# Performance work log

Hardware: AMD Instinct MI355X
Metric: run time of the kernel (lower is better)

## Reference

```python
import jax, jax.numpy as jnp
import numpy as np

V, D, L, ITERS, B, S = 30522, 256, 4, 10, 256, 512
UPDATE_RATE = 0.1


def _lin(x, w, b):
    # torch nn.Linear: y = x @ W^T + b, w: [out, in]
    return jnp.matmul(x, w.T) + b


def setup_inputs() -> dict:
    key = jax.random.key(0)
    ks = jax.random.split(key, 20)
    s = 0.02
    inp = {
        "input_ids": jax.random.randint(ks[0], (B, S), 0, V),
        "embedding": jax.random.normal(ks[1], (V, D), jnp.float32) * s,
        "pos_enc": jax.random.normal(ks[2], (1, S, D), jnp.float32) * s,
        # stacked per-layer PredictiveCodingLayer params [L, ...]
        "init_w": jax.random.normal(ks[3], (L, D, D), jnp.float32) * s,
        "init_b": jnp.zeros((L, D), jnp.float32),
        "pred_w": jax.random.normal(ks[4], (L, D, D), jnp.float32) * s,
        "pred_b": jnp.zeros((L, D), jnp.float32),
        "upd_w": jax.random.normal(ks[5], (L, D, D), jnp.float32) * s,
        "upd_b": jnp.zeros((L, D), jnp.float32),
        "start_q_w": jax.random.normal(ks[6], (D, D), jnp.float32) * s,
        "start_q_b": jnp.zeros((D,), jnp.float32),
        "end_q_w": jax.random.normal(ks[7], (D, D), jnp.float32) * s,
        "end_q_b": jnp.zeros((D,), jnp.float32),
        "key_w": jax.random.normal(ks[8], (D, D), jnp.float32) * s,
        "key_b": jnp.zeros((D,), jnp.float32),
        "ans_w1": jax.random.normal(ks[9], (D // 2, D), jnp.float32) * s,
        "ans_b1": jnp.zeros((D // 2,), jnp.float32),
        "ans_w2": jax.random.normal(ks[10], (2, D // 2), jnp.float32) * s,
        "ans_b2": jnp.zeros((2,), jnp.float32),
    }
    return inp


def reference(input_ids, embedding, pos_enc, init_w, init_b, pred_w, pred_b,
              upd_w, upd_b, start_q_w, start_q_b, end_q_w, end_q_b,
              key_w, key_b, ans_w1, ans_b1, ans_w2, ans_b2):
    seq_len = input_ids.shape[1]
    embeds = embedding[input_ids] + pos_enc[:, :seq_len, :]   # [B,S,D]
    pooled = jnp.mean(embeds, axis=1)                          # [B,D]

    predict = lambda i, r: _lin(r, pred_w[i], pred_b[i])

    # init_representation: tanh(Linear(x)) chained across layers
    reps = []
    cur = pooled
    for i in range(L):
        cur = jnp.tanh(_lin(cur, init_w[i], init_b[i]))
        reps.append(cur)
    ff_output = reps[-1]

    # iterative predictive-coding refinement
    for _ in range(ITERS):
        errors = [pooled - predict(0, reps[0])]
        for i in range(1, L):
            errors.append(jax.lax.stop_gradient(reps[i - 1]) - predict(i, reps[i]))
        new_reps = []
        for i in range(L):
            if i < L - 1:  # bidirectional
                error_above = reps[i] - predict(i + 1, reps[i + 1])
            else:
                error_above = jnp.zeros_like(reps[i])
            total_error = errors[i] + 0.5 * error_above
            # update: rep + rate * tanh(Linear(error))
            new_reps.append(reps[i] + UPDATE_RATE * jnp.tanh(_lin(total_error, upd_w[i], upd_b[i])))
        reps = new_reps

    refined = reps[-1] + ff_output                             # [B,D]
    token_keys = _lin(embeds, key_w, key_b)                    # [B,S,D]
    start_q = _lin(refined, start_q_w, start_q_b)
    end_q = _lin(refined, end_q_w, end_q_b)
    start_logits = jnp.einsum('bd,bsd->bs', start_q, token_keys)
    end_logits = jnp.einsum('bd,bsd->bs', end_q, token_keys)
    h = jax.nn.gelu(_lin(refined, ans_w1, ans_b1), approximate=False)
    answerable_logits = _lin(h, ans_w2, ans_b2)                # [B,2]
    return (start_logits, end_logits, answerable_logits)
```

## Files before the change

kernel.cpp:

```cpp
#include <hip/hip_runtime.h>
#include <math.h>

#define NB 256
#define NS 512
#define ND 256
#define NL 4
#define NITERS 10
#define DD (ND*ND)
#define BSTR 780
#define ASTR 132

__global__ __launch_bounds__(256) void k_pool1(const int* __restrict__ ids,
                                               const float* __restrict__ emb,
                                               const float* __restrict__ pos,
                                               float* __restrict__ partial) {
    const int bid = blockIdx.x;
    const int b = bid >> 2, q = bid & 3;
    const int t = threadIdx.x;
    __shared__ int sid[128];
    if (t < 128) sid[t] = ids[b * NS + q * 128 + t];
    __syncthreads();
    float acc = 0.f;
#pragma unroll 8
    for (int s = 0; s < 128; ++s)
        acc += emb[(size_t)sid[s] * ND + t] + pos[(q * 128 + s) * ND + t];
    partial[bid * ND + t] = acc;
}

__global__ __launch_bounds__(256) void k_prep(
    const float* __restrict__ pred_w, const float* __restrict__ pred_b,
    const float* __restrict__ upd_w,  const float* __restrict__ upd_b,
    const float* __restrict__ init_w,
    const float* __restrict__ sw, const float* __restrict__ sb,
    const float* __restrict__ ew, const float* __restrict__ eb,
    const float* __restrict__ kw, const float* __restrict__ kb,
    const float* __restrict__ w1,
    const float* __restrict__ partial,
    float* __restrict__ CM, float* __restrict__ CMI,
    float* __restrict__ KSt, float* __restrict__ KEt, float* __restrict__ W1t,
    float* __restrict__ cvec, float* __restrict__ rc0,
    float* __restrict__ vsk, float* __restrict__ vse,
    float* __restrict__ ksb, float* __restrict__ keb, float* __restrict__ scal)
{
    const int bid = blockIdx.x;
    const int t = threadIdx.x;

    if (bid < 576 || (bid >= 1056 && bid < 1120)) {
        int id, tile;
        if (bid < 576) { id = bid >> 6; tile = bid & 63; }
        else           { id = 9;        tile = bid - 1056; }
        const float* Asrc = nullptr; const float* Bsrc = nullptr;
        float alpha = 1.f, tau = 0.f; float* outp = nullptr;
        bool bT = false, aPool = false;
        switch (id) {
            case 0: Asrc = pred_w;        Bsrc = upd_w;        alpha=-1.f;  tau=0.5f; outp = CM + 0*(size_t)DD; break;
            case 1: Asrc = pred_w + DD;   Bsrc = upd_w;        alpha=-0.5f;           outp = CM + 1*(size_t)DD; break;
            case 2: Asrc = pred_w + DD;   Bsrc = upd_w + DD;   alpha=-1.f;  tau=0.5f; outp = CM + 4*(size_t)DD; break;
            case 3: Asrc = pred_w + 2*DD; Bsrc = upd_w + DD;   alpha=-0.5f;           outp = CM + 5*(size_t)DD; break;
            case 4: Asrc = pred_w + 2*DD; Bsrc = upd_w + 2*DD; alpha=-1.f;  tau=0.5f; outp = CM + 7*(size_t)DD; break;
            case 5: Asrc = pred_w + 3*DD; Bsrc = upd_w + 2*DD; alpha=-0.5f;           outp = CM + 8*(size_t)DD; break;
            case 6: Asrc = pred_w + 3*DD; Bsrc = upd_w + 3*DD; alpha=-1.f;            outp = CM + 10*(size_t)DD; break;
            case 7: Asrc = sw; Bsrc = kw; bT = true; outp = KSt; break;
            case 8: Asrc = ew; Bsrc = kw; bT = true; outp = KEt; break;
            default: Bsrc = upd_w; aPool = true; outp = rc0; break;
        }
        const float* Tsrc = (tau != 0.f) ? Bsrc : nullptr;
        const int i0 = (tile >> 3) * 32, j0 = (tile & 7) * 32;
        __shared__ float As[32 * 33];
        __shared__ float Bs[32 * 33];
        const int tx = t & 15, ty = t >> 4;
        float a00 = 0.f, a01 = 0.f, a10 = 0.f, a11 = 0.f;
        for (int e0 = 0; e0 < 256; e0 += 32) {
            __syncthreads();
            if (!aPool) {
                const int ii = t & 31, e8 = t >> 5;
#pragma unroll
                for (int p = 0; p < 4; ++p) {
                    int ee = e8 + 8 * p;
                    As[ee * 33 + ii] = Asrc[(size_t)(e0 + ee) * 256 + i0 + ii];
                }
            } else {
                const int ee = t & 31, i8 = t >> 5;
#pragma unroll
                for (int p = 0; p < 4; ++p) {
                    int ii = i8 + 8 * p;
                    const float* pp = partial + (size_t)(i0 + ii) * 4 * 256 + e0 + ee;
                    As[ee * 33 + ii] = (pp[0] + pp[256] + pp[512] + pp[768]) * (1.f / 512.f);
                }
            }
            if (!bT) {
                const int ee = t & 31, j8 = t >> 5;
#pragma unroll
                for (int p = 0; p < 4; ++p) {
                    int jj = j8 + 8 * p;
                    Bs[ee * 33 + jj] = Bsrc[(size_t)(j0 + jj) * 256 + e0 + ee];
                }
            } else {
                const int jj = t & 31, e8 = t >> 5;
#pragma unroll
                for (int p = 0; p < 4; ++p) {
                    int ee = e8 + 8 * p;
                    Bs[ee * 33 + jj] = Bsrc[(size_t)(e0 + ee) * 256 + j0 + jj];
                }
            }
            __syncthreads();
#pragma unroll
            for (int e = 0; e < 32; ++e) {
                float va0 = As[e * 33 + 2 * ty], va1 = As[e * 33 + 2 * ty + 1];
                float vb0 = Bs[e * 33 + 2 * tx], vb1 = Bs[e * 33 + 2 * tx + 1];
                a00 += va0 * vb0; a01 += va0 * vb1;
                a10 += va1 * vb0; a11 += va1 * vb1;
            }
        }
        float t00 = 0.f, t01 = 0.f, t10 = 0.f, t11 = 0.f;
        if (Tsrc) {
            t00 = Tsrc[(size_t)(j0 + 2 * tx) * 256 + i0 + 2 * ty];
            t01 = Tsrc[(size_t)(j0 + 2 * tx + 1) * 256 + i0 + 2 * ty];
            t10 = Tsrc[(size_t)(j0 + 2 * tx) * 256 + i0 + 2 * ty + 1];
            t11 = Tsrc[(size_t)(j0 + 2 * tx + 1) * 256 + i0 + 2 * ty + 1];
        }
        outp[(size_t)(i0 + 2 * ty) * 256 + j0 + 2 * tx]         = alpha * a00 + tau * t00;
        outp[(size_t)(i0 + 2 * ty) * 256 + j0 + 2 * tx + 1]     = alpha * a01 + tau * t01;
        outp[(size_t)(i0 + 2 * ty + 1) * 256 + j0 + 2 * tx]     = alpha * a10 + tau * t10;
        outp[(size_t)(i0 + 2 * ty + 1) * 256 + j0 + 2 * tx + 1] = alpha * a11 + tau * t11;
        return;
    }

    if (bid < 1024) {
        const int tid = bid - 576;
        const int m = tid >> 6, tile = tid & 63;
        const float* src; float* dst;
        if (m < 3) { src = upd_w + (size_t)(m + 1) * DD; dst = CM + (size_t)(3 + 3 * m) * DD; }
        else       { src = init_w + (size_t)(m - 3) * DD; dst = CMI + (size_t)(m - 3) * DD; }
        const int r0 = (tile >> 3) * 32, c0 = (tile & 7) * 32;
        __shared__ float T[32 * 33];
        const int cc = t & 31, r8 = t >> 5;
#pragma unroll
        for (int p = 0; p < 4; ++p) {
            int rr = r8 + 8 * p;
            T[rr * 33 + cc] = src[(size_t)(r0 + rr) * 256 + c0 + cc];
        }
        __syncthreads();
#pragma unroll
        for (int p = 0; p < 4; ++p) {
            int rr = r8 + 8 * p;
            dst[(size_t)(c0 + rr) * 256 + r0 + cc] = T[cc * 33 + rr];
        }
        return;
    }

    if (bid < 1056) {
        const int tile = bid - 1024;
        const int e0 = (tile >> 2) * 32, j0 = (tile & 3) * 32;
        __shared__ float T[32 * 33];
        const int cc = t & 31, r8 = t >> 5;
#pragma unroll
        for (int p = 0; p < 4; ++p) {
            int jj = r8 + 8 * p;
            T[jj * 33 + cc] = w1[(size_t)(j0 + jj) * 256 + e0 + cc];
        }
        __syncthreads();
#pragma unroll
        for (int p = 0; p < 4; ++p) {
            int ee = r8 + 8 * p;
            W1t[(size_t)(e0 + ee) * 128 + j0 + cc] = T[cc * 33 + ee];
        }
        return;
    }

    const int vb = bid - 1120;
    if (vb < 4) {
        const int l = vb;
        __shared__ float v[256];
        v[t] = (l < 3) ? pred_b[l * 256 + t] + 0.5f * pred_b[(l + 1) * 256 + t]
                       : pred_b[3 * 256 + t];
        __syncthreads();
        const float* U = upd_w + (size_t)l * DD + (size_t)t * 256;
        float acc = 0.f;
#pragma unroll 8
        for (int k = 0; k < 256; k += 4) {
            float4 u = *(const float4*)&U[k];
            acc += u.x * v[k] + u.y * v[k + 1] + u.z * v[k + 2] + u.w * v[k + 3];
        }
        cvec[l * 256 + t] = upd_b[l * 256 + t] - acc;
        return;
    }
    {
        const float* W = (vb == 4) ? sw : ew;
        const float* bb = (vb == 4) ? sb : eb;
        float* vout = (vb == 4) ? vsk : vse;
        float* bout = (vb == 4) ? ksb : keb;
        __shared__ float kbv[256], bbv[256], red[256];
        kbv[t] = kb[t]; bbv[t] = bb[t];
        __syncthreads();
        float a1 = 0.f, a2 = 0.f;
#pragma unroll 4
        for (int k = 0; k < 256; ++k) {
            a1 += W[(size_t)k * 256 + t] * kbv[k];
            a2 += kw[(size_t)k * 256 + t] * bbv[k];
        }
        vout[t] = a1; bout[t] = a2;
        red[t] = kbv[t] * bbv[t];
        __syncthreads();
        for (int s = 128; s > 0; s >>= 1) {
            if (t < s) red[t] += red[t + s];
            __syncthreads();
        }
        if (t == 0) scal[vb - 4] = red[0];
        return;
    }
}

__global__ __launch_bounds__(256) void k_init(const float* __restrict__ partial,
                                              const float* __restrict__ CMI,
                                              const float* __restrict__ init_b,
                                              float* __restrict__ rA,
                                              float* __restrict__ ff)
{
    const int row = blockIdx.x, t = threadIdx.x;
    __shared__ float xs[256];
    {
        const float* p = partial + (size_t)row * 4 * 256 + t;
        xs[t] = (p[0] + p[256] + p[512] + p[768]) * (1.f / 512.f);
    }
    float* rrow = rA + (size_t)row * 1024;
    for (int il = 0; il < 4; ++il) {
        __syncthreads();
        const float* M = CMI + (size_t)il * DD + t;
        float a0 = 0.f, a1 = 0.f, a2 = 0.f, a3 = 0.f;
#pragma unroll 8
        for (int k = 0; k < 256; k += 4) {
            float4 xv = *(const float4*)&xs[k];
            a0 += M[(size_t)(k + 0) * 256] * xv.x;
            a1 += M[(size_t)(k + 1) * 256] * xv.y;
            a2 += M[(size_t)(k + 2) * 256] * xv.z;
            a3 += M[(size_t)(k + 3) * 256] * xv.w;
        }
        float vx = tanhf(a0 + a1 + a2 + a3 + init_b[il * 256 + t]);
        __syncthreads();
        xs[t] = vx;
        rrow[il * 256 + t] = vx;
        if (il == 3) ff[(size_t)row * 256 + t] = vx;
    }
}

__global__ __launch_bounds__(256) void k_stage(const float* __restrict__ rcur,
                                               const float* __restrict__ CM,
                                               const float* __restrict__ cvec,
                                               const float* __restrict__ rc0,
                                               float* __restrict__ rnxt)
{
    __shared__ float Bs[32 * BSTR];
    __shared__ float As[4 * 8 * ASTR];
    const int bid = blockIdx.x;
    const int t = threadIdx.x;
    const int rowtile = bid >> 5, cg = bid & 31;
    const int l = cg >> 3, dbase = (cg & 7) * 32;
    const int slo = (l == 0) ? 0 : (l - 1);
    const int nj = (l == 0 || l == 3) ? 2 : 3;
    const int KK = nj * 256;
    const int nch = KK >> 7;
    const int r0 = rowtile * 32;
    const int slotBase = l * 3;

    {
        const int c8 = t & 7, col4 = c8 * 4;
        const int kq = ((t >> 3) + c8) & 31;
        const float* src = CM + (size_t)slotBase * DD + dbase + col4;
        for (int kb0 = kq * 4; kb0 < KK; kb0 += 128) {
            float4 v0 = *(const float4*)&src[(size_t)(kb0 + 0) * 256];
            float4 v1 = *(const float4*)&src[(size_t)(kb0 + 1) * 256];
            float4 v2 = *(const float4*)&src[(size_t)(kb0 + 2) * 256];
            float4 v3 = *(const float4*)&src[(size_t)(kb0 + 3) * 256];
            *(float4*)&Bs[(col4 + 0) * BSTR + kb0] = make_float4(v0.x, v1.x, v2.x, v3.x);
            *(float4*)&Bs[(col4 + 1) * BSTR + kb0] = make_float4(v0.y, v1.y, v2.y, v3.y);
            *(float4*)&Bs[(col4 + 2) * BSTR + kb0] = make_float4(v0.z, v1.z, v2.z, v3.z);
            *(float4*)&Bs[(col4 + 3) * BSTR + kb0] = make_float4(v0.w, v1.w, v2.w, v3.w);
        }
    }
    __syncthreads();

    const int wv = t >> 6, lane = t & 63;
    const int arow = lane >> 3, af = lane & 7;
    const int cpair = lane & 3, ks = lane >> 2;
    const int krot = (ks + 2 * cpair) & 15;
    float* Aw = As + wv * (8 * ASTR);

    float acc[8][8];
#pragma unroll
    for (int i = 0; i < 8; ++i)
#pragma unroll
        for (int j = 0; j < 8; ++j) acc[i][j] = 0.f;

    const float* aSrc = rcur + (size_t)(r0 + wv * 8 + arow) * 1024 + slo * 256;

    float4 pa0 = *(const float4*)&aSrc[af * 4];
    float4 pa1 = *(const float4*)&aSrc[af * 4 + 32];
    float4 pa2 = *(const float4*)&aSrc[af * 4 + 64];
    float4 pa3 = *(const float4*)&aSrc[af * 4 + 96];

    for (int c = 0; c < nch; ++c) {
        *(float4*)&Aw[arow * ASTR + af * 4]      = pa0;
        *(float4*)&Aw[arow * ASTR + af * 4 + 32] = pa1;
        *(float4*)&Aw[arow * ASTR + af * 4 + 64] = pa2;
        *(float4*)&Aw[arow * ASTR + af * 4 + 96] = pa3;
        if (c + 1 < nch) {
            const int kg = (c + 1) * 128;
            pa0 = *(const float4*)&aSrc[kg + af * 4];
            pa1 = *(const float4*)&aSrc[kg + af * 4 + 32];
            pa2 = *(const float4*)&aSrc[kg + af * 4 + 64];
            pa3 = *(const float4*)&aSrc[kg + af * 4 + 96];
        }
#pragma unroll
        for (int h = 0; h < 2; ++h) {
            float4 ar[8], bc[8];
            const int ka = h * 64 + krot * 4;
            const int kb = c * 128 + h * 64 + krot * 4;
#pragma unroll
            for (int rr = 0; rr < 8; ++rr)
                ar[rr] = *(const float4*)&Aw[rr * ASTR + ka];
#pragma unroll
            for (int cc = 0; cc < 8; ++cc)
                bc[cc] = *(const float4*)&Bs[(cpair * 8 + cc) * BSTR + kb];
#pragma unroll
            for (int rr = 0; rr < 8; ++rr)
#pragma unroll
                for (int cc = 0; cc < 8; ++cc)
                    acc[rr][cc] += ar[rr].x * bc[cc].x + ar[rr].y * bc[cc].y
                                 + ar[rr].z * bc[cc].z + ar[rr].w * bc[cc].w;
        }
    }

#pragma unroll
    for (int rr = 0; rr < 8; ++rr)
#pragma unroll
        for (int cc = 0; cc < 8; ++cc) {
            float v = acc[rr][cc];
            v += __shfl_xor(v, 4);
            v += __shfl_xor(v, 8);
            acc[rr][cc] = v;
        }

    if ((lane & 12) == 0) {
        const int ksg = lane >> 4;
        float* w = Aw + ((ksg * 4 + cpair) << 6);
#pragma unroll
        for (int rr = 0; rr < 8; ++rr) {
            *(float4*)&w[rr * 8]     = make_float4(acc[rr][0], acc[rr][1], acc[rr][2], acc[rr][3]);
            *(float4*)&w[rr * 8 + 4] = make_float4(acc[rr][4], acc[rr][5], acc[rr][6], acc[rr][7]);
        }
    }
    {
        const int out_rr = lane >> 3, out_cc4 = (lane >> 2) & 1, out_cp = lane & 3;
        const int off = out_rr * 8 + out_cc4 * 4;
        float4 s0 = *(const float4*)&Aw[((0 * 4 + out_cp) << 6) + off];
        float4 s1 = *(const float4*)&Aw[((1 * 4 + out_cp) << 6) + off];
        float4 s2 = *(const float4*)&Aw[((2 * 4 + out_cp) << 6) + off];
        float4 s3 = *(const float4*)&Aw[((3 * 4 + out_cp) << 6) + off];
        float z0 = s0.x + s1.x + s2.x + s3.x;
        float z1 = s0.y + s1.y + s2.y + s3.y;
        float z2 = s0.z + s1.z + s2.z + s3.z;
        float z3 = s0.w + s1.w + s2.w + s3.w;

        const int grow = r0 + wv * 8 + out_rr;
        const int dcol = dbase + out_cp * 8 + out_cc4 * 4;
        float4 cv = *(const float4*)&cvec[l * 256 + dcol];
        z0 += cv.x; z1 += cv.y; z2 += cv.z; z3 += cv.w;
        if (l == 0) {
            float4 rc = *(const float4*)&rc0[(size_t)grow * 256 + dcol];
            z0 += rc.x; z1 += rc.y; z2 += rc.z; z3 += rc.w;
        }
        float4 rold = *(const float4*)&rcur[(size_t)grow * 1024 + l * 256 + dcol];
        float4 o;
        o.x = rold.x + 0.1f * tanhf(z0);
        o.y = rold.y + 0.1f * tanhf(z1);
        o.z = rold.z + 0.1f * tanhf(z2);
        o.w = rold.w + 0.1f * tanhf(z3);
        *(float4*)&rnxt[(size_t)grow * 1024 + l * 256 + dcol] = o;
    }
}

__global__ __launch_bounds__(256) void k_heads(const float* __restrict__ rA,
    const float* __restrict__ ff,
    const float* __restrict__ KSt, const float* __restrict__ KEt,
    const float* __restrict__ ksb, const float* __restrict__ keb,
    const float* __restrict__ vsk, const float* __restrict__ vse,
    const float* __restrict__ scal,
    const float* __restrict__ W1t, const float* __restrict__ b1,
    const float* __restrict__ w2, const float* __restrict__ b2,
    float* __restrict__ sqk, float* __restrict__ eqk,
    float* __restrict__ sqb, float* __restrict__ eqb,
    float* __restrict__ out)
{
    const int row = blockIdx.x, t = threadIdx.x;
    __shared__ float xs[256];
    __shared__ float red[256];
    __shared__ float hp[256];
    __shared__ float hs[128];
    xs[t] = rA[(size_t)row * 1024 + 768 + t] + ff[(size_t)row * 256 + t];
    __syncthreads();
    {
        float a0 = 0.f, a1 = 0.f, a2 = 0.f, a3 = 0.f;
        float e0 = 0.f, e1 = 0.f, e2 = 0.f, e3 = 0.f;
        const float* KS = KSt + t;
        const float* KE = KEt + t;
#pragma unroll 4
        for (int f = 0; f < 256; f += 4) {
            float4 xv = *(const float4*)&xs[f];
            a0 += KS[(size_t)(f + 0) * 256] * xv.x; a1 += KS[(size_t)(f + 1) * 256] * xv.y;
            a2 += KS[(size_t)(f + 2) * 256] * xv.z; a3 += KS[(size_t)(f + 3) * 256] * xv.w;
            e0 += KE[(size_t)(f + 0) * 256] * xv.x; e1 += KE[(size_t)(f + 1) * 256] * xv.y;
            e2 += KE[(size_t)(f + 2) * 256] * xv.z; e3 += KE[(size_t)(f + 3) * 256] * xv.w;
        }
        sqk[(size_t)row * 256 + t] = a0 + a1 + a2 + a3 + ksb[t];
        eqk[(size_t)row * 256 + t] = e0 + e1 + e2 + e3 + keb[t];
    }
    red[t] = vsk[t] * xs[t];
    __syncthreads();
    for (int s = 128; s > 0; s >>= 1) { if (t < s) red[t] += red[t + s]; __syncthreads(); }
    if (t == 0) sqb[row] = red[0] + scal[0];
    __syncthreads();
    red[t] = vse[t] * xs[t];
    __syncthreads();
    for (int s = 128; s > 0; s >>= 1) { if (t < s) red[t] += red[t + s]; __syncthreads(); }
    if (t == 0) eqb[row] = red[0] + scal[1];
    __syncthreads();
    {
        const int j = t & 127, half = t >> 7;
        float a = 0.f;
        const float* W = W1t + (size_t)half * 128 * 128 + j;
        const float* xh = &xs[half * 128];
#pragma unroll 8
        for (int e = 0; e < 128; ++e) a += W[(size_t)e * 128] * xh[e];
        hp[half * 128 + j] = a;
    }
    __syncthreads();
    if (t < 128) {
        float x = hp[t] + hp[128 + t] + b1[t];
        hs[t] = 0.5f * x * (1.f + erff(x * 0.70710678118654752f));
    }
    __syncthreads();
    if (t < 128) { red[t] = hs[t] * w2[t]; red[128 + t] = hs[t] * w2[128 + t]; }
    __syncthreads();
    for (int s = 64; s > 0; s >>= 1) {
        if (t < s) red[t] += red[t + s];
        else if (t >= 128 && t < 128 + s) red[t] += red[t + s];
        __syncthreads();
    }
    if (t == 0)   out[2 * NB * NS + row * 2 + 0] = red[0] + b2[0];
    if (t == 128) out[2 * NB * NS + row * 2 + 1] = red[128] + b2[1];
}

__global__ __launch_bounds__(512) void k_logits(const int* __restrict__ ids,
                                                const float* __restrict__ emb,
                                                const float* __restrict__ pos,
                                                const float* __restrict__ sqk,
                                                const float* __restrict__ eqk,
                                                const float* __restrict__ sqb,
                                                const float* __restrict__ eqb,
                                                float* __restrict__ out) {
    const int bid = blockIdx.x;
    const int b = bid >> 2, q = bid & 3;
    const int t = threadIdx.x;
    __shared__ float sk[ND], ek[ND];
    __shared__ int sid[128];
    if (t < 256) sk[t] = sqk[b * ND + t];
    else ek[t - 256] = eqk[b * ND + t - 256];
    if (t < 128) sid[t] = ids[b * NS + q * 128 + t];
    __syncthreads();
    const int w = t >> 6, lane = t & 63;
    const float4 ks = *(const float4*)&sk[4 * lane];
    const float4 ke = *(const float4*)&ek[4 * lane];
    const float qbs = sqb[b], qbe = eqb[b];
    for (int si = w; si < 128; si += 8) {
        const int s = q * 128 + si;
        const int id = sid[si];
        const float4 e4 = *(const float4*)&emb[(size_t)id * ND + 4 * lane];
        const float4 p4 = *(const float4*)&pos[s * ND + 4 * lane];
        float vx = e4.x + p4.x, vy = e4.y + p4.y, vz = e4.z + p4.z, vw = e4.w + p4.w;
        float ds = vx * ks.x + vy * ks.y + vz * ks.z + vw * ks.w;
        float de = vx * ke.x + vy * ke.y + vz * ke.z + vw * ke.w;
#pragma unroll
        for (int off = 32; off >= 1; off >>= 1) {
            ds += __shfl_xor(ds, off);
            de += __shfl_xor(de, off);
        }
        if (lane == 0) {
            out[b * NS + s] = ds + qbs;
            out[NB * NS + b * NS + s] = de + qbe;
        }
    }
}

extern "C" void kernel_launch(void* const* d_in, const int* in_sizes, int n_in,
                              void* d_out, int out_size, void* d_ws, size_t ws_size,
                              hipStream_t stream) {
    const int*   ids    = (const int*)d_in[0];
    const float* emb    = (const float*)d_in[1];
    const float* pos    = (const float*)d_in[2];
    const float* init_w = (const float*)d_in[3];
    const float* init_b = (const float*)d_in[4];
    const float* pred_w = (const float*)d_in[5];
    const float* pred_b = (const float*)d_in[6];
    const float* upd_w  = (const float*)d_in[7];
    const float* upd_b  = (const float*)d_in[8];
    const float* sw     = (const float*)d_in[9];
    const float* sb     = (const float*)d_in[10];
    const float* ew     = (const float*)d_in[11];
    const float* eb     = (const float*)d_in[12];
    const float* kw     = (const float*)d_in[13];
    const float* kb     = (const float*)d_in[14];
    const float* w1     = (const float*)d_in[15];
    const float* b1     = (const float*)d_in[16];
    const float* w2     = (const float*)d_in[17];
    const float* b2     = (const float*)d_in[18];
    float* out = (float*)d_out;

    float* ws = (float*)d_ws;
    float* partial = ws;                 ws += 1024 * 256;
    float* rA      = ws;                 ws += 256 * 1024;
    float* rB      = ws;                 ws += 256 * 1024;
    float* ff      = ws;                 ws += 256 * 256;
    float* CM      = ws;                 ws += 12 * DD;
    float* CMI     = ws;                 ws += 4 * DD;
    float* KSt     = ws;                 ws += DD;
    float* KEt     = ws;                 ws += DD;
    float* W1t     = ws;                 ws += 256 * 128;
    float* cvec    = ws;                 ws += 4 * 256;
    float* rc0     = ws;                 ws += 256 * 256;
    float* vsk     = ws;                 ws += 256;
    float* vse     = ws;                 ws += 256;
    float* ksb     = ws;                 ws += 256;
    float* keb     = ws;                 ws += 256;
    float* scal    = ws;                 ws += 8;
    float* sqk     = ws;                 ws += 256 * 256;
    float* eqk     = ws;                 ws += 256 * 256;
    float* sqb     = ws;                 ws += 256;
    float* eqb     = ws;                 ws += 256;

    k_pool1<<<1024, 256, 0, stream>>>(ids, emb, pos, partial);

    k_prep<<<1126, 256, 0, stream>>>(pred_w, pred_b, upd_w, upd_b, init_w,
                                     sw, sb, ew, eb, kw, kb, w1, partial,
                                     CM, CMI, KSt, KEt, W1t,
                                     cvec, rc0, vsk, vse, ksb, keb, scal);

    k_init<<<256, 256, 0, stream>>>(partial, CMI, init_b, rA, ff);

    float* cur = rA;
    float* nxt = rB;
    for (int it = 0; it < NITERS; ++it) {
        k_stage<<<256, 256, 0, stream>>>(cur, CM, cvec, rc0, nxt);
        float* tmp = cur; cur = nxt; nxt = tmp;
    }

    k_heads<<<256, 256, 0, stream>>>(rA, ff, KSt, KEt, ksb, keb, vsk, vse, scal,
                                     W1t, b1, w2, b2, sqk, eqk, sqb, eqb, out);

    k_logits<<<1024, 512, 0, stream>>>(ids, emb, pos, sqk, eqk, sqb, eqb, out);
}
```

Before: 234.3 us.

## Fuse refinement iterations into one cooperative persistent kernel with per-rowgroup barriers

Replaces ten separate stage-kernel launches with a single cooperative kernel that loops over the iterations. The weight tile is staged into LDS once and reused across all iterations. Blocks are synchronized per 32-row group through atomic counters that k_init zeroes. This removes launch gaps and repeated weight loads, at the cost of spin-wait barriers and a reliance on all blocks being co-resident.

```diff
diff --git a/kernel.cpp b/kernel.cpp
--- a/kernel.cpp
+++ b/kernel.cpp
@@ -215,9 +215,11 @@
                                               const float* __restrict__ CMI,
                                               const float* __restrict__ init_b,
                                               float* __restrict__ rA,
-                                              float* __restrict__ ff)
+                                              float* __restrict__ ff,
+                                              unsigned int* __restrict__ cnt)
 {
     const int row = blockIdx.x, t = threadIdx.x;
+    if (row == 0) cnt[t] = 0u;
     __shared__ float xs[256];
     {
         const float* p = partial + (size_t)row * 4 * 256 + t;
@@ -244,23 +246,25 @@
     }
 }
 
-__global__ __launch_bounds__(256) void k_stage(const float* __restrict__ rcur,
-                                               const float* __restrict__ CM,
-                                               const float* __restrict__ cvec,
-                                               const float* __restrict__ rc0,
-                                               float* __restrict__ rnxt)
+__global__ __launch_bounds__(256) void k_refine(float* __restrict__ bufA,
+                                                float* __restrict__ bufB,
+                                                const float* __restrict__ CM,
+                                                const float* __restrict__ cvec,
+                                                const float* __restrict__ rc0,
+                                                unsigned int* __restrict__ cnt)
 {
     __shared__ float Bs[32 * BSTR];
     __shared__ float As[4 * 8 * ASTR];
     const int bid = blockIdx.x;
     const int t = threadIdx.x;
-    const int rowtile = bid >> 5, cg = bid & 31;
+    const int grp = bid & 7;
+    const int cg = bid >> 3;
     const int l = cg >> 3, dbase = (cg & 7) * 32;
     const int slo = (l == 0) ? 0 : (l - 1);
     const int nj = (l == 0 || l == 3) ? 2 : 3;
     const int KK = nj * 256;
     const int nch = KK >> 7;
-    const int r0 = rowtile * 32;
+    const int r0 = grp * 32;
     const int slotBase = l * 3;
 
     {
@@ -286,97 +290,114 @@
     const int krot = (ks + 2 * cpair) & 15;
     float* Aw = As + wv * (8 * ASTR);
 
-    float acc[8][8];
-#pragma unroll
-    for (int i = 0; i < 8; ++i)
-#pragma unroll
-        for (int j = 0; j < 8; ++j) acc[i][j] = 0.f;
-
-    const float* aSrc = rcur + (size_t)(r0 + wv * 8 + arow) * 1024 + slo * 256;
-
-    float4 pa0 = *(const float4*)&aSrc[af * 4];
-    float4 pa1 = *(const float4*)&aSrc[af * 4 + 32];
-    float4 pa2 = *(const float4*)&aSrc[af * 4 + 64];
-    float4 pa3 = *(const float4*)&aSrc[af * 4 + 96];
-
-    for (int c = 0; c < nch; ++c) {
-        *(float4*)&Aw[arow * ASTR + af * 4]      = pa0;
-        *(float4*)&Aw[arow * ASTR + af * 4 + 32] = pa1;
-        *(float4*)&Aw[arow * ASTR + af * 4 + 64] = pa2;
-        *(float4*)&Aw[arow * ASTR + af * 4 + 96] = pa3;
-        if (c + 1 < nch) {
-            const int kg = (c + 1) * 128;
-            pa0 = *(const float4*)&aSrc[kg + af * 4];
-            pa1 = *(const float4*)&aSrc[kg + af * 4 + 32];
-            pa2 = *(const float4*)&aSrc[kg + af * 4 + 64];
-            pa3 = *(const float4*)&aSrc[kg + af * 4 + 96];
-        }
-#pragma unroll
-        for (int h = 0; h < 2; ++h) {
-            float4 ar[8], bc[8];
-            const int ka = h * 64 + krot * 4;
-            const int kb = c * 128 + h * 64 + krot * 4;
-#pragma unroll
-            for (int rr = 0; rr < 8; ++rr)
-                ar[rr] = *(const float4*)&Aw[rr * ASTR + ka];
-#pragma unroll
-            for (int cc = 0; cc < 8; ++cc)
-                bc[cc] = *(const float4*)&Bs[(cpair * 8 + cc) * BSTR + kb];
-#pragma unroll
-            for (int rr = 0; rr < 8; ++rr)
+    float* rcur = bufA;
+    float* rnxt = bufB;
+
+    for (int it = 0; it < NITERS; ++it) {
+        float acc[8][8];
+#pragma unroll
+        for (int i = 0; i < 8; ++i)
+#pragma unroll
+            for (int j = 0; j < 8; ++j) acc[i][j] = 0.f;
+
+        const float* aSrc = rcur + (size_t)(r0 + wv * 8 + arow) * 1024 + slo * 256;
+        float4 pa0 = *(const float4*)&aSrc[af * 4];
+        float4 pa1 = *(const float4*)&aSrc[af * 4 + 32];
+        float4 pa2 = *(const float4*)&aSrc[af * 4 + 64];
+        float4 pa3 = *(const float4*)&aSrc[af * 4 + 96];
+
+        for (int c = 0; c < nch; ++c) {
+            *(float4*)&Aw[arow * ASTR + af * 4]      = pa0;
+            *(float4*)&Aw[arow * ASTR + af * 4 + 32] = pa1;
+            *(float4*)&Aw[arow * ASTR + af * 4 + 64] = pa2;
+            *(float4*)&Aw[arow * ASTR + af * 4 + 96] = pa3;
+            if (c + 1 < nch) {
+                const int kg = (c + 1) * 128;
+                pa0 = *(const float4*)&aSrc[kg + af * 4];
+                pa1 = *(const float4*)&aSrc[kg + af * 4 + 32];
+                pa2 = *(const float4*)&aSrc[kg + af * 4 + 64];
+                pa3 = *(const float4*)&aSrc[kg + af * 4 + 96];
+            }
+#pragma unroll
+            for (int h = 0; h < 2; ++h) {
+                float4 ar[8], bc[8];
+                const int ka = h * 64 + krot * 4;
+                const int kb = c * 128 + h * 64 + krot * 4;
+#pragma unroll
+                for (int rr = 0; rr < 8; ++rr)
+                    ar[rr] = *(const float4*)&Aw[rr * ASTR + ka];
 #pragma unroll
                 for (int cc = 0; cc < 8; ++cc)
-                    acc[rr][cc] += ar[rr].x * bc[cc].x + ar[rr].y * bc[cc].y
-                                 + ar[rr].z * bc[cc].z + ar[rr].w * bc[cc].w;
-        }
-    }
-
-#pragma unroll
-    for (int rr = 0; rr < 8; ++rr)
-#pragma unroll
-        for (int cc = 0; cc < 8; ++cc) {
-            float v = acc[rr][cc];
-            v += __shfl_xor(v, 4);
-            v += __shfl_xor(v, 8);
-            acc[rr][cc] = v;
-        }
-
-    if ((lane & 12) == 0) {
-        const int ksg = lane >> 4;
-        float* w = Aw + ((ksg * 4 + cpair) << 6);
-#pragma unroll
-        for (int rr = 0; rr < 8; ++rr) {
-            *(float4*)&w[rr * 8]     = make_float4(acc[rr][0], acc[rr][1], acc[rr][2], acc[rr][3]);
-            *(float4*)&w[rr * 8 + 4] = make_float4(acc[rr][4], acc[rr][5], acc[rr][6], acc[rr][7]);
-        }
-    }
-    {
-        const int out_rr = lane >> 3, out_cc4 = (lane >> 2) & 1, out_cp = lane & 3;
-        const int off = out_rr * 8 + out_cc4 * 4;
-        float4 s0 = *(const float4*)&Aw[((0 * 4 + out_cp) << 6) + off];
-        float4 s1 = *(const float4*)&Aw[((1 * 4 + out_cp) << 6) + off];
-        float4 s2 = *(const float4*)&Aw[((2 * 4 + out_cp) << 6) + off];
-        float4 s3 = *(const float4*)&Aw[((3 * 4 + out_cp) << 6) + off];
-        float z0 = s0.x + s1.x + s2.x + s3.x;
-        float z1 = s0.y + s1.y + s2.y + s3.y;
-        float z2 = s0.z + s1.z + s2.z + s3.z;
-        float z3 = s0.w + s1.w + s2.w + s3.w;
-
-        const int grow = r0 + wv * 8 + out_rr;
-        const int dcol = dbase + out_cp * 8 + out_cc4 * 4;
-        float4 cv = *(const float4*)&cvec[l * 256 + dcol];
-        z0 += cv.x; z1 += cv.y; z2 += cv.z; z3 += cv.w;
-        if (l == 0) {
-            float4 rc = *(const float4*)&rc0[(size_t)grow * 256 + dcol];
-            z0 += rc.x; z1 += rc.y; z2 += rc.z; z3 += rc.w;
-        }
-        float4 rold = *(const float4*)&rcur[(size_t)grow * 1024 + l * 256 + dcol];
-        float4 o;
-        o.x = rold.x + 0.1f * tanhf(z0);
-        o.y = rold.y + 0.1f * tanhf(z1);
-        o.z = rold.z + 0.1f * tanhf(z2);
-        o.w = rold.w + 0.1f * tanhf(z3);
-        *(float4*)&rnxt[(size_t)grow * 1024 + l * 256 + dcol] = o;
+                    bc[cc] = *(const float4*)&Bs[(cpair * 8 + cc) * BSTR + kb];
+#pragma unroll
+                for (int rr = 0; rr < 8; ++rr)
+#pragma unroll
+                    for (int cc = 0; cc < 8; ++cc)
+                        acc[rr][cc] += ar[rr].x * bc[cc].x + ar[rr].y * bc[cc].y
+                                     + ar[rr].z * bc[cc].z + ar[rr].w * bc[cc].w;
+            }
+        }
+
+#pragma unroll
+        for (int rr = 0; rr < 8; ++rr)
+#pragma unroll
+            for (int cc = 0; cc < 8; ++cc) {
+                float v = acc[rr][cc];
+                v += __shfl_xor(v, 4);
+                v += __shfl_xor(v, 8);
+                acc[rr][cc] = v;
+            }
+        if ((lane & 12) == 0) {
+            const int ksg = lane >> 4;
+            float* w = Aw + ((ksg * 4 + cpair) << 6);
+#pragma unroll
+            for (int rr = 0; rr < 8; ++rr) {
+                *(float4*)&w[rr * 8]     = make_float4(acc[rr][0], acc[rr][1], acc[rr][2], acc[rr][3]);
+                *(float4*)&w[rr * 8 + 4] = make_float4(acc[rr][4], acc[rr][5], acc[rr][6], acc[rr][7]);
+            }
+        }
+        {
+            const int out_rr = lane >> 3, out_cc4 = (lane >> 2) & 1, out_cp = lane & 3;
+            const int off = out_rr * 8 + out_cc4 * 4;
+            float4 s0 = *(const float4*)&Aw[((0 * 4 + out_cp) << 6) + off];
+            float4 s1 = *(const float4*)&Aw[((1 * 4 + out_cp) << 6) + off];
+            float4 s2 = *(const float4*)&Aw[((2 * 4 + out_cp) << 6) + off];
+            float4 s3 = *(const float4*)&Aw[((3 * 4 + out_cp) << 6) + off];
+            float z0 = s0.x + s1.x + s2.x + s3.x;
+            float z1 = s0.y + s1.y + s2.y + s3.y;
+            float z2 = s0.z + s1.z + s2.z + s3.z;
+            float z3 = s0.w + s1.w + s2.w + s3.w;
+
+            const int grow = r0 + wv * 8 + out_rr;
+            const int dcol = dbase + out_cp * 8 + out_cc4 * 4;
+            float4 cv = *(const float4*)&cvec[l * 256 + dcol];
+            z0 += cv.x; z1 += cv.y; z2 += cv.z; z3 += cv.w;
+            if (l == 0) {
+                float4 rc = *(const float4*)&rc0[(size_t)grow * 256 + dcol];
+                z0 += rc.x; z1 += rc.y; z2 += rc.z; z3 += rc.w;
+            }
+            float4 rold = *(const float4*)&rcur[(size_t)grow * 1024 + l * 256 + dcol];
+            float4 o;
+            o.x = rold.x + 0.1f * tanhf(z0);
+            o.y = rold.y + 0.1f * tanhf(z1);
+            o.z = rold.z + 0.1f * tanhf(z2);
+            o.w = rold.w + 0.1f * tanhf(z3);
+            *(float4*)&rnxt[(size_t)grow * 1024 + l * 256 + dcol] = o;
+        }
+
+        if (it < NITERS - 1) {
+            __syncthreads();
+            __threadfence();
+            __syncthreads();
+            if (t == 0) {
+                unsigned int* c = &cnt[grp * 32 + it];
+                atomicAdd(c, 1u);
+                while (atomicAdd(c, 0u) < 32u) __builtin_amdgcn_s_sleep(1);
+            }
+            __syncthreads();
+            __threadfence();
+        }
+        float* tmp = rcur; rcur = rnxt; rnxt = tmp;
     }
 }
 
@@ -537,6 +558,7 @@
     float* eqk     = ws;                 ws += 256 * 256;
     float* sqb     = ws;                 ws += 256;
     float* eqb     = ws;                 ws += 256;
+    unsigned int* cnt = (unsigned int*)ws; ws += 256;
 
     k_pool1<<<1024, 256, 0, stream>>>(ids, emb, pos, partial);
 
@@ -545,13 +567,13 @@
                                      CM, CMI, KSt, KEt, W1t,
                                      cvec, rc0, vsk, vse, ksb, keb, scal);
 
-    k_init<<<256, 256, 0, stream>>>(partial, CMI, init_b, rA, ff);
-
-    float* cur = rA;
-    float* nxt = rB;
-    for (int it = 0; it < NITERS; ++it) {
-        k_stage<<<256, 256, 0, stream>>>(cur, CM, cvec, rc0, nxt);
-        float* tmp = cur; cur = nxt; nxt = tmp;
+    k_init<<<256, 256, 0, stream>>>(partial, CMI, init_b, rA, ff, cnt);
+
+    {
+        void* args[] = { (void*)&rA, (void*)&rB, (void*)&CM,
+                         (void*)&cvec, (void*)&rc0, (void*)&cnt };
+        hipLaunchCooperativeKernel((void*)k_refine, dim3(256), dim3(256),
+                                   args, 0, stream);
     }
 
     k_heads<<<256, 256, 0, stream>>>(rA, ff, KSt, KEt, ksb, keb, vsk, vse, scal,
```

Result: slower. 514.0 us (+119.4%).
